# Kernel optimization log

Measured on AMD Instinct MI355X. Metric: run time of the kernel, lower is better.

## Reference

```python
import jax, jax.numpy as jnp
import numpy as np

B, S, E, D, H, DH, FF = 16, 512, 128, 768, 12, 64, 3072
EPS = 1e-12


def _ln(x, g, b):
    m = jnp.mean(x, axis=-1, keepdims=True)
    v = jnp.var(x, axis=-1, keepdims=True)
    return (x - m) * jax.lax.rsqrt(v + EPS) * g + b


def setup_inputs() -> dict:
    key = jax.random.key(0)
    ks = jax.random.split(key, 24)
    w = lambda k, shp: (jax.random.normal(k, shp, jnp.float32) * 0.02)
    inp = {
        "word_hidden_states": jax.random.normal(ks[0], (B, S, D), jnp.float32),
        "entity_hidden_states": jax.random.normal(ks[1], (B, E, D), jnp.float32),
        "attention_mask": jnp.zeros((B, 1, 1, S + E), jnp.float32),
        # attention projections (used as x @ W + b)
        "W_q": w(ks[2], (D, D)), "b_q": jnp.zeros((D,), jnp.float32),
        "W_k": w(ks[3], (D, D)), "b_k": jnp.zeros((D,), jnp.float32),
        "W_v": w(ks[4], (D, D)), "b_v": jnp.zeros((D,), jnp.float32),
        "W_w2e": w(ks[5], (D, D)), "b_w2e": jnp.zeros((D,), jnp.float32),
        "W_e2w": w(ks[6], (D, D)), "b_e2w": jnp.zeros((D,), jnp.float32),
        "W_e2e": w(ks[7], (D, D)), "b_e2e": jnp.zeros((D,), jnp.float32),
        # BertSelfOutput
        "W_ao": w(ks[8], (D, D)), "b_ao": jnp.zeros((D,), jnp.float32),
        "g_ao": jnp.ones((D,), jnp.float32), "beta_ao": jnp.zeros((D,), jnp.float32),
        # BertIntermediate / BertOutput
        "W_i": w(ks[9], (D, FF)), "b_i": jnp.zeros((FF,), jnp.float32),
        "W_o": w(ks[10], (FF, D)), "b_o": jnp.zeros((D,), jnp.float32),
        "g_o": jnp.ones((D,), jnp.float32), "beta_o": jnp.zeros((D,), jnp.float32),
    }
    return inp


def _split_heads(x):
    b, t, _ = x.shape
    return x.reshape(b, t, H, DH)  # [B,T,H,DH]


def reference(word_hidden_states, entity_hidden_states, attention_mask,
              W_q, b_q, W_k, b_k, W_v, b_v,
              W_w2e, b_w2e, W_e2w, b_e2w, W_e2e, b_e2e,
              W_ao, b_ao, g_ao, beta_ao,
              W_i, b_i, W_o, b_o, g_o, beta_o):
    word_size = word_hidden_states.shape[1]
    kv_in = jnp.concatenate([word_hidden_states, entity_hidden_states], axis=1)  # [B,S+E,D]

    q_ww = _split_heads(word_hidden_states @ W_q + b_q)
    q_we = _split_heads(word_hidden_states @ W_w2e + b_w2e)
    q_ew = _split_heads(entity_hidden_states @ W_e2w + b_e2w)
    q_ee = _split_heads(entity_hidden_states @ W_e2e + b_e2e)

    k_all = _split_heads(kv_in @ W_k + b_k)
    v_all = _split_heads(kv_in @ W_v + b_v)
    k_w, k_e = k_all[:, :word_size], k_all[:, word_size:]

    dot = lambda q, k: jnp.einsum('bqhd,bkhd->bhqk', q, k)
    top = jnp.concatenate([dot(q_ww, k_w), dot(q_we, k_e)], axis=-1)  # [B,H,S,S+E]
    bot = jnp.concatenate([dot(q_ew, k_w), dot(q_ee, k_e)], axis=-1)  # [B,H,E,S+E]
    scores = jnp.concatenate([top, bot], axis=-2)  # [B,H,S+E,S+E]
    scores = scores / np.sqrt(DH).astype(np.float32) + attention_mask
    probs = jax.nn.softmax(scores, axis=-1)

    ctx = jnp.einsum('bhqk,bkhd->bqhd', probs, v_all).reshape(kv_in.shape[0], -1, D)

    ao = _ln(ctx @ W_ao + b_ao + kv_in, g_ao, beta_ao)
    inter = jax.nn.gelu(ao @ W_i + b_i, approximate=False)
    out = _ln(inter @ W_o + b_o + ao, g_o, beta_o)
    return out[:, :word_size, :], out[:, word_size:, :]
```

## Files before the change

### kernel.cpp

```cpp
#include <hip/hip_runtime.h>
#include <stdint.h>


#define B_ 16
#define S_ 512
#define E_ 128
#define T_ 640
#define D_ 768
#define H_ 12
#define DH_ 64
#define FF_ 3072
#define SCP_LD 664

typedef unsigned short u16;
typedef __bf16 bf16x8 __attribute__((ext_vector_type(8)));
typedef u16 u16x8 __attribute__((ext_vector_type(8)));
typedef u16 u16x4 __attribute__((ext_vector_type(4)));
typedef float f32x4 __attribute__((ext_vector_type(4)));

__device__ __forceinline__ float b2f(u16 v) {
  unsigned u = ((unsigned)v) << 16;
  return __builtin_bit_cast(float, u);
}
__device__ __forceinline__ u16 f2b(float f) {
  unsigned u = __builtin_bit_cast(unsigned, f);
  u += 0x7FFFu + ((u >> 16) & 1u);
  return (u16)(u >> 16);
}

__device__ __forceinline__ void gl_lds16(const u16* g, u16* l) {
  __builtin_amdgcn_global_load_lds((__attribute__((address_space(1))) const void*)g,
                                   (__attribute__((address_space(3))) void*)l, 16, 0, 0);
}

template <int EPI>
__global__ __launch_bounds__(256) void gemm_kernel(
    const u16* __restrict__ A, const u16* __restrict__ Bt0,
    const u16* __restrict__ Bt1, const u16* __restrict__ bias0,
    const u16* __restrict__ bias1, int msel, u16* __restrict__ C,
    int lda, int ldc, int K, long long sA, long long sC) {
  __shared__ __align__(16) u16 As[128 * 32];
  __shared__ __align__(16) u16 Bs[128 * 32];

  const int tid = threadIdx.x;
  const int m0 = blockIdx.x * 128, n0 = blockIdx.y * 128;
  const u16* Bt = (blockIdx.x >= msel) ? Bt1 : Bt0;
  const u16* bias = (blockIdx.x >= msel) ? bias1 : bias0;
  A += (long long)blockIdx.z * sA + (long long)m0 * lda;
  Bt += (long long)n0 * K;
  C += (long long)blockIdx.z * sC;

  const int lane = tid & 63, wave = tid >> 6;
  const int wm = (wave & 1) << 6, wn = (wave >> 1) << 6;
  const int l15 = lane & 15, quad = lane >> 4;

  const int r0 = tid >> 2, c0 = (tid & 3) << 3;
  const u16* ga0 = A + (long long)r0 * lda + c0;
  const u16* ga1 = A + (long long)(r0 + 64) * lda + c0;
  const u16* gb0 = Bt + (long long)r0 * K + c0;
  const u16* gb1 = Bt + (long long)(r0 + 64) * K + c0;

  f32x4 acc[4][4] = {};

  for (int k0 = 0; k0 < K; k0 += 32) {
    __syncthreads();
    gl_lds16(ga0 + k0, &As[tid * 8]);
    gl_lds16(ga1 + k0, &As[2048 + tid * 8]);
    gl_lds16(gb0 + k0, &Bs[tid * 8]);
    gl_lds16(gb1 + k0, &Bs[2048 + tid * 8]);
    __syncthreads();

    bf16x8 af[4], bfr[4];
#pragma unroll
    for (int i = 0; i < 4; i++)
      af[i] = *(const bf16x8*)&As[(wm + i * 16 + l15) * 32 + quad * 8];
#pragma unroll
    for (int i = 0; i < 4; i++)
      bfr[i] = *(const bf16x8*)&Bs[(wn + i * 16 + l15) * 32 + quad * 8];
#pragma unroll
    for (int i = 0; i < 4; i++)
#pragma unroll
      for (int j = 0; j < 4; j++)
        acc[i][j] = __builtin_amdgcn_mfma_f32_16x16x32_bf16(af[i], bfr[j], acc[i][j], 0, 0, 0);
  }

  float bv[4];
#pragma unroll
  for (int j = 0; j < 4; j++) bv[j] = b2f(bias[n0 + wn + j * 16 + l15]);

  if (EPI == 2) {
#pragma unroll
    for (int i = 0; i < 4; i++) {
      const int grow = m0 + wm + i * 16 + quad * 4;
      const int bb = grow / T_, tt = grow - bb * T_;
#pragma unroll
      for (int j = 0; j < 4; j++) {
        const int col = n0 + wn + j * 16 + l15;
        u16x4 pk;
#pragma unroll
        for (int r = 0; r < 4; r++) pk[r] = f2b(acc[i][j][r] + bv[j]);
        *(u16x4*)&C[(((long long)bb * H_ + (col >> 6)) * DH_ + (col & 63)) * T_ + tt] = pk;
      }
    }
  } else {
#pragma unroll
    for (int i = 0; i < 4; i++) {
      const int row = m0 + wm + i * 16 + quad * 4;
#pragma unroll
      for (int j = 0; j < 4; j++) {
        const int col = n0 + wn + j * 16 + l15;
#pragma unroll
        for (int r = 0; r < 4; r++) {
          float v = acc[i][j][r] + bv[j];
          if (EPI == 1) v = 0.5f * v * (1.0f + erff(v * 0.70710678118654752f));
          C[(long long)(row + r) * ldc + col] = f2b(v);
        }
      }
    }
  }
}

__global__ __launch_bounds__(256) void attn_kernel(
    const u16* __restrict__ Qw, const u16* __restrict__ Qe,
    const u16* __restrict__ Kb, const u16* __restrict__ Vt,
    const float* __restrict__ mask, u16* __restrict__ ctx) {
  const int q0 = blockIdx.x * 32;
  const int h = blockIdx.y, b = blockIdx.z;

  __shared__ __align__(16) u16 scp[32 * SCP_LD];
  __shared__ float rsum[32];

  const int tid = threadIdx.x;
  const int lane = tid & 63, wave = tid >> 6;
  const int l15 = lane & 15, quad = lane >> 4;

  const long long bh = (long long)b * T_ * D_ + h * DH_;
  const long long bhV = ((long long)b * H_ + h) * DH_ * T_;

  bf16x8 qf[2][2][2];
#pragma unroll
  for (int g = 0; g < 2; g++) {
    const u16* qwp = Qw + bh + (long long)(q0 + g * 16 + l15) * D_ + quad * 8;
    const u16* qep = Qe + bh + (long long)(q0 + g * 16 + l15) * D_ + quad * 8;
    qf[g][0][0] = *(const bf16x8*)(qwp);
    qf[g][0][1] = *(const bf16x8*)(qwp + 32);
    qf[g][1][0] = *(const bf16x8*)(qep);
    qf[g][1][1] = *(const bf16x8*)(qep + 32);
  }

#pragma unroll
  for (int i = 0; i < 10; i++) {
    const int key0 = wave * 160 + i * 16;
    const u16* kp = Kb + bh + (long long)(key0 + l15) * D_ + quad * 8;
    const bf16x8 kf0 = *(const bf16x8*)(kp);
    const bf16x8 kf1 = *(const bf16x8*)(kp + 32);
    const float mv = mask[b * T_ + key0 + l15];
    const int e = (key0 < S_) ? 0 : 1;
#pragma unroll
    for (int g = 0; g < 2; g++) {
      f32x4 a = {0.f, 0.f, 0.f, 0.f};
      a = __builtin_amdgcn_mfma_f32_16x16x32_bf16(qf[g][e][0], kf0, a, 0, 0, 0);
      a = __builtin_amdgcn_mfma_f32_16x16x32_bf16(qf[g][e][1], kf1, a, 0, 0, 0);
#pragma unroll
      for (int r = 0; r < 4; r++)
        scp[(g * 16 + quad * 4 + r) * SCP_LD + key0 + l15] = f2b(a[r] * 0.125f + mv);
    }
  }
  __syncthreads();

  {
    const int row = tid >> 3, ck = tid & 7;
    float mx = -1e30f;
#pragma unroll
    for (int c = 0; c < 10; c++) {
      const u16x8 v = *(const u16x8*)&scp[row * SCP_LD + c * 64 + ck * 8];
#pragma unroll
      for (int e = 0; e < 8; e++) mx = fmaxf(mx, b2f(v[e]));
    }
#pragma unroll
    for (int d = 4; d; d >>= 1) mx = fmaxf(mx, __shfl_xor(mx, d, 8));
    float sum = 0.f;
#pragma unroll
    for (int c = 0; c < 10; c++) {
      u16* p = &scp[row * SCP_LD + c * 64 + ck * 8];
      const u16x8 v = *(const u16x8*)p;
      u16x8 o;
#pragma unroll
      for (int e = 0; e < 8; e++) {
        const float ex = __expf(b2f(v[e]) - mx);
        sum += ex;
        o[e] = f2b(ex);
      }
      *(u16x8*)p = o;
    }
#pragma unroll
    for (int d = 4; d; d >>= 1) sum += __shfl_xor(sum, d, 8);
    if (ck == 0) rsum[row] = sum;
  }
  __syncthreads();

  f32x4 o0 = {0.f, 0.f, 0.f, 0.f}, o1 = {0.f, 0.f, 0.f, 0.f};
  const u16* vrow = Vt + bhV + (long long)(wave * 16 + l15) * T_;
#pragma unroll
  for (int kc = 0; kc < T_; kc += 64) {
#pragma unroll
    for (int ks = 0; ks < 2; ks++) {
      const int ko = kc + ks * 32 + quad * 8;
      const bf16x8 vf = *(const bf16x8*)(vrow + ko);
      const bf16x8 p0 = *(const bf16x8*)&scp[l15 * SCP_LD + ko];
      const bf16x8 p1 = *(const bf16x8*)&scp[(16 + l15) * SCP_LD + ko];
      o0 = __builtin_amdgcn_mfma_f32_16x16x32_bf16(p0, vf, o0, 0, 0, 0);
      o1 = __builtin_amdgcn_mfma_f32_16x16x32_bf16(p1, vf, o1, 0, 0, 0);
    }
  }

  u16* cp0 = ctx + bh + (long long)(q0 + quad * 4) * D_ + wave * 16 + l15;
#pragma unroll
  for (int r = 0; r < 4; r++) cp0[(long long)r * D_] = f2b(o0[r] / rsum[quad * 4 + r]);
  u16* cp1 = ctx + bh + (long long)(q0 + 16 + quad * 4) * D_ + wave * 16 + l15;
#pragma unroll
  for (int r = 0; r < 4; r++) cp1[(long long)r * D_] = f2b(o1[r] / rsum[16 + quad * 4 + r]);
}

template <int SPLIT>
__global__ __launch_bounds__(256) void ln_kernel(
    const u16* __restrict__ x, const u16* __restrict__ res,
    const u16* __restrict__ g, const u16* __restrict__ beta,
    void* __restrict__ out_) {
  const int row = blockIdx.x;
  const int tid = threadIdx.x;
  const u16* xp = x + (long long)row * D_;
  const u16* rp = res + (long long)row * D_;
  float v[3], s = 0.f, s2 = 0.f;
#pragma unroll
  for (int i = 0; i < 3; i++) {
    const int c = tid + i * 256;
    v[i] = b2f(xp[c]) + b2f(rp[c]);
    s += v[i];
    s2 += v[i] * v[i];
  }
#pragma unroll
  for (int d = 32; d; d >>= 1) {
    s += __shfl_xor(s, d, 64);
    s2 += __shfl_xor(s2, d, 64);
  }
  __shared__ float red[8];
  const int wave = tid >> 6;
  if ((tid & 63) == 0) { red[wave * 2] = s; red[wave * 2 + 1] = s2; }
  __syncthreads();
  s = red[0] + red[2] + red[4] + red[6];
  s2 = red[1] + red[3] + red[5] + red[7];
  const float mean = s * (1.f / 768.f);
  const float var = s2 * (1.f / 768.f) - mean * mean;
  const float rs = rsqrtf(var + 1e-12f);
  if (SPLIT) {
    float* out = (float*)out_;
    const int b = row / T_, t = row % T_;
    float* op = (t < S_) ? out + ((long long)b * S_ + t) * D_
                         : out + (long long)B_ * S_ * D_ + ((long long)b * E_ + (t - S_)) * D_;
#pragma unroll
    for (int i = 0; i < 3; i++) {
      const int c = tid + i * 256;
      op[c] = (v[i] - mean) * rs * b2f(g[c]) + b2f(beta[c]);
    }
  } else {
    u16* op = (u16*)out_ + (long long)row * D_;
#pragma unroll
    for (int i = 0; i < 3; i++) {
      const int c = tid + i * 256;
      op[c] = f2b((v[i] - mean) * rs * b2f(g[c]) + b2f(beta[c]));
    }
  }
}

__global__ __launch_bounds__(256) void transpose_kernel(
    const float* __restrict__ in, u16* __restrict__ out, int K, int N) {
  __shared__ u16 t[32][33];
  const int n0 = blockIdx.x * 32, k0 = blockIdx.y * 32;
  const int tx = threadIdx.x, ty = threadIdx.y;
#pragma unroll
  for (int i = 0; i < 4; i++)
    t[ty + i * 8][tx] = f2b(in[(long long)(k0 + ty + i * 8) * N + n0 + tx]);
  __syncthreads();
#pragma unroll
  for (int i = 0; i < 4; i++)
    out[(long long)(n0 + ty + i * 8) * K + k0 + tx] = t[tx][ty + i * 8];
}

struct T7 { const float* s[7]; u16* d[7]; };
__global__ __launch_bounds__(256) void transpose7_kernel(T7 a) {
  __shared__ u16 t[32][33];
  const float* in = a.s[blockIdx.z];
  u16* out = a.d[blockIdx.z];
  const int n0 = blockIdx.x * 32, k0 = blockIdx.y * 32;
  const int tx = threadIdx.x, ty = threadIdx.y;
#pragma unroll
  for (int i = 0; i < 4; i++)
    t[ty + i * 8][tx] = f2b(in[(long long)(k0 + ty + i * 8) * 768 + n0 + tx]);
  __syncthreads();
#pragma unroll
  for (int i = 0; i < 4; i++)
    out[(long long)(n0 + ty + i * 8) * 768 + k0 + tx] = t[tx][ty + i * 8];
}

__global__ __launch_bounds__(256) void concat_kernel(
    const float* __restrict__ w, const float* __restrict__ e, u16* __restrict__ x) {
  const long long i = (long long)(blockIdx.x * 256 + threadIdx.x) * 8;
  const long long NW = (long long)B_ * S_ * D_;
  const long long NE = (long long)B_ * E_ * D_;
  const long long SD = (long long)S_ * D_;
  const long long ED = (long long)E_ * D_;
  const long long TD = (long long)T_ * D_;
  const float* src;
  u16* dst;
  if (i < NW) {
    const long long b = i / SD, r = i % SD;
    src = w + i;
    dst = &x[b * TD + r];
  } else {
    const long long j = i - NW;
    if (j >= NE) return;
    const long long b = j / ED, r = j % ED;
    src = e + j;
    dst = &x[b * TD + SD + r];
  }
  const float4 f0 = *(const float4*)(src);
  const float4 f1 = *(const float4*)(src + 4);
  u16x8 o;
  o[0] = f2b(f0.x); o[1] = f2b(f0.y); o[2] = f2b(f0.z); o[3] = f2b(f0.w);
  o[4] = f2b(f1.x); o[5] = f2b(f1.y); o[6] = f2b(f1.z); o[7] = f2b(f1.w);
  *(u16x8*)dst = o;
}

struct CvtArgs { const float* src[13]; u16* dst[13]; int n[13]; };
__global__ __launch_bounds__(256) void cvt_vecs_kernel(CvtArgs a) {
  const int v = blockIdx.x;
  const float* s = a.src[v];
  u16* d = a.dst[v];
  const int n = a.n[v];
  for (int i = threadIdx.x; i < n; i += 256) d[i] = f2b(s[i]);
}

extern "C" void kernel_launch(void* const* d_in, const int* in_sizes, int n_in,
                              void* d_out, int out_size, void* d_ws, size_t ws_size,
                              hipStream_t stream) {
  (void)in_sizes; (void)n_in; (void)out_size; (void)ws_size;
  const float* word = (const float*)d_in[0];
  const float* ent = (const float*)d_in[1];
  const float* mask = (const float*)d_in[2];
  const float* W_q = (const float*)d_in[3];
  const float* b_q = (const float*)d_in[4];
  const float* W_k = (const float*)d_in[5];
  const float* b_k = (const float*)d_in[6];
  const float* W_v = (const float*)d_in[7];
  const float* b_v = (const float*)d_in[8];
  const float* W_w2e = (const float*)d_in[9];
  const float* b_w2e = (const float*)d_in[10];
  const float* W_e2w = (const float*)d_in[11];
  const float* b_e2w = (const float*)d_in[12];
  const float* W_e2e = (const float*)d_in[13];
  const float* b_e2e = (const float*)d_in[14];
  const float* W_ao = (const float*)d_in[15];
  const float* b_ao = (const float*)d_in[16];
  const float* g_ao = (const float*)d_in[17];
  const float* be_ao = (const float*)d_in[18];
  const float* W_i = (const float*)d_in[19];
  const float* b_i = (const float*)d_in[20];
  const float* W_o = (const float*)d_in[21];
  const float* b_o = (const float*)d_in[22];
  const float* g_o = (const float*)d_in[23];
  const float* be_o = (const float*)d_in[24];

  const size_t DD = (size_t)D_ * D_ * 2;
  const size_t DFF = (size_t)D_ * FF_ * 2;
  const size_t TD = (size_t)B_ * T_ * D_ * 2;
  size_t off = 0;
  char* base = (char*)d_ws;
  auto take = [&](size_t n) { void* p = base + off; off += n; return p; };
  u16* wqT = (u16*)take(DD);
  u16* wkT = (u16*)take(DD);
  u16* wvT = (u16*)take(DD);
  u16* ww2eT = (u16*)take(DD);
  u16* we2wT = (u16*)take(DD);
  u16* we2eT = (u16*)take(DD);
  u16* waoT = (u16*)take(DD);
  u16* wiT = (u16*)take(DFF);
  u16* woT = (u16*)take(DFF);
  u16* vecs = (u16*)take(2 * 16384);
  u16* xall = (u16*)take(TD);
  u16* qw = (u16*)take(TD);
  u16* qe = (u16*)take(TD);
  u16* kb = (u16*)take(TD);
  u16* vt = (u16*)take(TD);
  u16* ctxb = (u16*)take(TD);
  u16* inter = (u16*)take((size_t)B_ * T_ * FF_ * 2);
  u16* bq = vecs + 0 * 768;
  u16* bk = vecs + 1 * 768;
  u16* bv = vecs + 2 * 768;
  u16* bw2e = vecs + 3 * 768;
  u16* be2w = vecs + 4 * 768;
  u16* be2e = vecs + 5 * 768;
  u16* bao = vecs + 6 * 768;
  u16* gao = vecs + 7 * 768;
  u16* beao = vecs + 8 * 768;
  u16* bo = vecs + 9 * 768;
  u16* go = vecs + 10 * 768;
  u16* beo = vecs + 11 * 768;
  u16* bi = vecs + 12 * 768;
  u16* ao_raw = qw;
  u16* ao = kb;
  u16* out_raw = qe;

  CvtArgs ca;
  ca.src[0] = b_q;   ca.dst[0] = bq;   ca.n[0] = 768;
  ca.src[1] = b_k;   ca.dst[1] = bk;   ca.n[1] = 768;
  ca.src[2] = b_v;   ca.dst[2] = bv;   ca.n[2] = 768;
  ca.src[3] = b_w2e; ca.dst[3] = bw2e; ca.n[3] = 768;
  ca.src[4] = b_e2w; ca.dst[4] = be2w; ca.n[4] = 768;
  ca.src[5] = b_e2e; ca.dst[5] = be2e; ca.n[5] = 768;
  ca.src[6] = b_ao;  ca.dst[6] = bao;  ca.n[6] = 768;
  ca.src[7] = g_ao;  ca.dst[7] = gao;  ca.n[7] = 768;
  ca.src[8] = be_ao; ca.dst[8] = beao; ca.n[8] = 768;
  ca.src[9] = b_o;   ca.dst[9] = bo;   ca.n[9] = 768;
  ca.src[10] = g_o;  ca.dst[10] = go;  ca.n[10] = 768;
  ca.src[11] = be_o; ca.dst[11] = beo; ca.n[11] = 768;
  ca.src[12] = b_i;  ca.dst[12] = bi;  ca.n[12] = 3072;
  cvt_vecs_kernel<<<13, 256, 0, stream>>>(ca);

  T7 t7;
  t7.s[0] = W_q;   t7.d[0] = wqT;
  t7.s[1] = W_k;   t7.d[1] = wkT;
  t7.s[2] = W_v;   t7.d[2] = wvT;
  t7.s[3] = W_w2e; t7.d[3] = ww2eT;
  t7.s[4] = W_e2w; t7.d[4] = we2wT;
  t7.s[5] = W_e2e; t7.d[5] = we2eT;
  t7.s[6] = W_ao;  t7.d[6] = waoT;
  const dim3 tb(32, 8);
  transpose7_kernel<<<dim3(24, 24, 7), tb, 0, stream>>>(t7);
  transpose_kernel<<<dim3(96, 24), tb, 0, stream>>>(W_i, wiT, 768, 3072);
  transpose_kernel<<<dim3(24, 96), tb, 0, stream>>>(W_o, woT, 3072, 768);
  concat_kernel<<<3840, 256, 0, stream>>>(word, ent, xall);

  const long long TDs = (long long)T_ * D_;
  const int BIG = 1 << 30;
  gemm_kernel<0><<<dim3(80, 6, 1), 256, 0, stream>>>(xall, wkT, wkT, bk, bk, BIG, kb, 768, 768, 768, 0, 0);
  gemm_kernel<2><<<dim3(80, 6, 1), 256, 0, stream>>>(xall, wvT, wvT, bv, bv, BIG, vt, 768, 0, 768, 0, 0);
  gemm_kernel<0><<<dim3(5, 6, 16), 256, 0, stream>>>(xall, wqT, we2wT, bq, be2w, 4, qw, 768, 768, 768, TDs, TDs);
  gemm_kernel<0><<<dim3(5, 6, 16), 256, 0, stream>>>(xall, ww2eT, we2eT, bw2e, be2e, 4, qe, 768, 768, 768, TDs, TDs);

  attn_kernel<<<dim3(20, 12, 16), 256, 0, stream>>>(qw, qe, kb, vt, mask, ctxb);

  gemm_kernel<0><<<dim3(80, 6, 1), 256, 0, stream>>>(ctxb, waoT, waoT, bao, bao, BIG, ao_raw, 768, 768, 768, 0, 0);
  ln_kernel<0><<<10240, 256, 0, stream>>>(ao_raw, xall, gao, beao, ao);
  gemm_kernel<1><<<dim3(80, 24, 1), 256, 0, stream>>>(ao, wiT, wiT, bi, bi, BIG, inter, 768, 3072, 768, 0, 0);
  gemm_kernel<0><<<dim3(80, 6, 1), 256, 0, stream>>>(inter, woT, woT, bo, bo, BIG, out_raw, 3072, 768, 3072, 0, 0);
  ln_kernel<1><<<10240, 256, 0, stream>>>(out_raw, ao, go, beo, d_out);
}
```

Measured before the change: 554.0 us.

## Merge QKV projection GEMMs into two launches and deepen K-step to 64

Measured after the change: 510.2 us. 7.9% less time.

```diff
diff --git a/kernel.cpp b/kernel.cpp
--- a/kernel.cpp
+++ b/kernel.cpp
@@ -33,23 +33,10 @@
                                    (__attribute__((address_space(3))) void*)l, 16, 0, 0);
 }
 
-template <int EPI>
-__global__ __launch_bounds__(256) void gemm_kernel(
-    const u16* __restrict__ A, const u16* __restrict__ Bt0,
-    const u16* __restrict__ Bt1, const u16* __restrict__ bias0,
-    const u16* __restrict__ bias1, int msel, u16* __restrict__ C,
-    int lda, int ldc, int K, long long sA, long long sC) {
-  __shared__ __align__(16) u16 As[128 * 32];
-  __shared__ __align__(16) u16 Bs[128 * 32];
-
+__device__ __forceinline__ void gemm_core(
+    const u16* __restrict__ A, const u16* __restrict__ Bt, int lda, int K,
+    u16* As, u16* Bs, f32x4 (&acc)[4][4]) {
   const int tid = threadIdx.x;
-  const int m0 = blockIdx.x * 128, n0 = blockIdx.y * 128;
-  const u16* Bt = (blockIdx.x >= msel) ? Bt1 : Bt0;
-  const u16* bias = (blockIdx.x >= msel) ? bias1 : bias0;
-  A += (long long)blockIdx.z * sA + (long long)m0 * lda;
-  Bt += (long long)n0 * K;
-  C += (long long)blockIdx.z * sC;
-
   const int lane = tid & 63, wave = tid >> 6;
   const int wm = (wave & 1) << 6, wn = (wave >> 1) << 6;
   const int l15 = lane & 15, quad = lane >> 4;
@@ -60,35 +47,109 @@
   const u16* gb0 = Bt + (long long)r0 * K + c0;
   const u16* gb1 = Bt + (long long)(r0 + 64) * K + c0;
 
-  f32x4 acc[4][4] = {};
-
-  for (int k0 = 0; k0 < K; k0 += 32) {
+  for (int k0 = 0; k0 < K; k0 += 64) {
     __syncthreads();
     gl_lds16(ga0 + k0, &As[tid * 8]);
     gl_lds16(ga1 + k0, &As[2048 + tid * 8]);
+    gl_lds16(ga0 + k0 + 32, &As[4096 + tid * 8]);
+    gl_lds16(ga1 + k0 + 32, &As[6144 + tid * 8]);
     gl_lds16(gb0 + k0, &Bs[tid * 8]);
     gl_lds16(gb1 + k0, &Bs[2048 + tid * 8]);
+    gl_lds16(gb0 + k0 + 32, &Bs[4096 + tid * 8]);
+    gl_lds16(gb1 + k0 + 32, &Bs[6144 + tid * 8]);
     __syncthreads();
 
-    bf16x8 af[4], bfr[4];
-#pragma unroll
-    for (int i = 0; i < 4; i++)
-      af[i] = *(const bf16x8*)&As[(wm + i * 16 + l15) * 32 + quad * 8];
-#pragma unroll
-    for (int i = 0; i < 4; i++)
-      bfr[i] = *(const bf16x8*)&Bs[(wn + i * 16 + l15) * 32 + quad * 8];
-#pragma unroll
-    for (int i = 0; i < 4; i++)
-#pragma unroll
-      for (int j = 0; j < 4; j++)
-        acc[i][j] = __builtin_amdgcn_mfma_f32_16x16x32_bf16(af[i], bfr[j], acc[i][j], 0, 0, 0);
-  }
-
+#pragma unroll
+    for (int p = 0; p < 2; p++) {
+      bf16x8 af[4], bfr[4];
+#pragma unroll
+      for (int i = 0; i < 4; i++)
+        af[i] = *(const bf16x8*)&As[p * 4096 + (wm + i * 16 + l15) * 32 + quad * 8];
+#pragma unroll
+      for (int i = 0; i < 4; i++)
+        bfr[i] = *(const bf16x8*)&Bs[p * 4096 + (wn + i * 16 + l15) * 32 + quad * 8];
+#pragma unroll
+      for (int i = 0; i < 4; i++)
+#pragma unroll
+        for (int j = 0; j < 4; j++)
+          acc[i][j] = __builtin_amdgcn_mfma_f32_16x16x32_bf16(af[i], bfr[j], acc[i][j], 0, 0, 0);
+    }
+  }
+}
+
+__device__ __forceinline__ void epi_store(
+    f32x4 (&acc)[4][4], const u16* __restrict__ bias, u16* __restrict__ C,
+    int m0, int n0, int ldc, bool gelu) {
+  const int tid = threadIdx.x;
+  const int lane = tid & 63, wave = tid >> 6;
+  const int wm = (wave & 1) << 6, wn = (wave >> 1) << 6;
+  const int l15 = lane & 15, quad = lane >> 4;
   float bv[4];
 #pragma unroll
   for (int j = 0; j < 4; j++) bv[j] = b2f(bias[n0 + wn + j * 16 + l15]);
-
-  if (EPI == 2) {
+#pragma unroll
+  for (int i = 0; i < 4; i++) {
+    const int row = m0 + wm + i * 16 + quad * 4;
+#pragma unroll
+    for (int j = 0; j < 4; j++) {
+      const int col = n0 + wn + j * 16 + l15;
+#pragma unroll
+      for (int r = 0; r < 4; r++) {
+        float v = acc[i][j][r] + bv[j];
+        if (gelu) v = 0.5f * v * (1.0f + erff(v * 0.70710678118654752f));
+        C[(long long)(row + r) * ldc + col] = f2b(v);
+      }
+    }
+  }
+}
+
+template <int MODE, bool GELU>
+__global__ __launch_bounds__(256) void gemm_kernel(
+    const u16* __restrict__ A, const u16* __restrict__ Bt0,
+    const u16* __restrict__ Bt1, const u16* __restrict__ Bt2,
+    const u16* __restrict__ Bt3, const u16* __restrict__ bias0,
+    const u16* __restrict__ bias1, const u16* __restrict__ bias2,
+    const u16* __restrict__ bias3, u16* __restrict__ C0, u16* __restrict__ C1,
+    int lda, int ldc, int K, long long sA, long long sC) {
+  __shared__ __align__(16) u16 As[8192];
+  __shared__ __align__(16) u16 Bs[8192];
+
+  const int m0 = blockIdx.x * 128;
+  int n0;
+  const u16 *Bt, *bias;
+  u16* C;
+  bool vstore = false;
+  if (MODE == 0) {
+    n0 = blockIdx.y * 128;
+    Bt = Bt0; bias = bias0; C = C0;
+  } else if (MODE == 1) {
+    if (blockIdx.y < 6) { n0 = blockIdx.y * 128; Bt = Bt0; bias = bias0; C = C0; }
+    else { n0 = (blockIdx.y - 6) * 128; Bt = Bt1; bias = bias1; C = C1; vstore = true; }
+  } else {
+    const bool isE = (blockIdx.x >= 4);
+    if (blockIdx.y < 6) {
+      n0 = blockIdx.y * 128;
+      Bt = isE ? Bt1 : Bt0; bias = isE ? bias1 : bias0; C = C0;
+    } else {
+      n0 = (blockIdx.y - 6) * 128;
+      Bt = isE ? Bt3 : Bt2; bias = isE ? bias3 : bias2; C = C1;
+    }
+  }
+
+  const u16* Ab = A + (long long)blockIdx.z * sA + (long long)m0 * lda;
+  C += (long long)blockIdx.z * sC;
+
+  f32x4 acc[4][4] = {};
+  gemm_core(Ab, Bt + (long long)n0 * K, lda, K, As, Bs, acc);
+
+  if (MODE == 1 && vstore) {
+    const int tid = threadIdx.x;
+    const int lane = tid & 63, wave = tid >> 6;
+    const int wm = (wave & 1) << 6, wn = (wave >> 1) << 6;
+    const int l15 = lane & 15, quad = lane >> 4;
+    float bv[4];
+#pragma unroll
+    for (int j = 0; j < 4; j++) bv[j] = b2f(bias[n0 + wn + j * 16 + l15]);
 #pragma unroll
     for (int i = 0; i < 4; i++) {
       const int grow = m0 + wm + i * 16 + quad * 4;
@@ -103,20 +164,7 @@
       }
     }
   } else {
-#pragma unroll
-    for (int i = 0; i < 4; i++) {
-      const int row = m0 + wm + i * 16 + quad * 4;
-#pragma unroll
-      for (int j = 0; j < 4; j++) {
-        const int col = n0 + wn + j * 16 + l15;
-#pragma unroll
-        for (int r = 0; r < 4; r++) {
-          float v = acc[i][j][r] + bv[j];
-          if (EPI == 1) v = 0.5f * v * (1.0f + erff(v * 0.70710678118654752f));
-          C[(long long)(row + r) * ldc + col] = f2b(v);
-        }
-      }
-    }
+    epi_store(acc, bias, C, m0, n0, ldc, GELU);
   }
 }
 
@@ -442,17 +490,24 @@
   concat_kernel<<<3840, 256, 0, stream>>>(word, ent, xall);
 
   const long long TDs = (long long)T_ * D_;
-  const int BIG = 1 << 30;
-  gemm_kernel<0><<<dim3(80, 6, 1), 256, 0, stream>>>(xall, wkT, wkT, bk, bk, BIG, kb, 768, 768, 768, 0, 0);
-  gemm_kernel<2><<<dim3(80, 6, 1), 256, 0, stream>>>(xall, wvT, wvT, bv, bv, BIG, vt, 768, 0, 768, 0, 0);
-  gemm_kernel<0><<<dim3(5, 6, 16), 256, 0, stream>>>(xall, wqT, we2wT, bq, be2w, 4, qw, 768, 768, 768, TDs, TDs);
-  gemm_kernel<0><<<dim3(5, 6, 16), 256, 0, stream>>>(xall, ww2eT, we2eT, bw2e, be2e, 4, qe, 768, 768, 768, TDs, TDs);
+  gemm_kernel<1, false><<<dim3(80, 12, 1), 256, 0, stream>>>(
+      xall, wkT, wvT, nullptr, nullptr, bk, bv, nullptr, nullptr, kb, vt,
+      768, 768, 768, 0, 0);
+  gemm_kernel<2, false><<<dim3(5, 12, 16), 256, 0, stream>>>(
+      xall, wqT, we2wT, ww2eT, we2eT, bq, be2w, bw2e, be2e, qw, qe,
+      768, 768, 768, TDs, TDs);
 
   attn_kernel<<<dim3(20, 12, 16), 256, 0, stream>>>(qw, qe, kb, vt, mask, ctxb);
 
-  gemm_kernel<0><<<dim3(80, 6, 1), 256, 0, stream>>>(ctxb, waoT, waoT, bao, bao, BIG, ao_raw, 768, 768, 768, 0, 0);
+  gemm_kernel<0, false><<<dim3(80, 6, 1), 256, 0, stream>>>(
+      ctxb, waoT, nullptr, nullptr, nullptr, bao, nullptr, nullptr, nullptr,
+      ao_raw, nullptr, 768, 768, 768, 0, 0);
   ln_kernel<0><<<10240, 256, 0, stream>>>(ao_raw, xall, gao, beao, ao);
-  gemm_kernel<1><<<dim3(80, 24, 1), 256, 0, stream>>>(ao, wiT, wiT, bi, bi, BIG, inter, 768, 3072, 768, 0, 0);
-  gemm_kernel<0><<<dim3(80, 6, 1), 256, 0, stream>>>(inter, woT, woT, bo, bo, BIG, out_raw, 3072, 768, 3072, 0, 0);
+  gemm_kernel<0, true><<<dim3(80, 24, 1), 256, 0, stream>>>(
+      ao, wiT, nullptr, nullptr, nullptr, bi, nullptr, nullptr, nullptr,
+      inter, nullptr, 768, 3072, 768, 0, 0);
+  gemm_kernel<0, false><<<dim3(80, 6, 1), 256, 0, stream>>>(
+      inter, woT, nullptr, nullptr, nullptr, bo, nullptr, nullptr, nullptr,
+      out_raw, nullptr, 3072, 768, 3072, 0, 0);
   ln_kernel<1><<<10240, 256, 0, stream>>>(out_raw, ao, go, beo, d_out);
 }
```
